# Kernel tuning notes

Measured on AMD Instinct MI355X. Metric: run time of the kernel, lower is better.

## Reference

```python
import jax, jax.numpy as jnp
import numpy as np

B = 524288
N = 5  # graph size hard-coded by reshape(batch, 5, 5) in the original
THRESHOLD = 0.85


def build_graph(x):
    # x: [B, N]. Row j of sample b is x[b] if x[b, j] != 0 else (1 - x[b]).
    # The torch code reads the condition from detached numpy values, so the
    # condition carries no gradient -> stop_gradient here.
    cond = jax.lax.stop_gradient(x)[:, :, None] != 0          # [B, N, 1]
    mat = jnp.where(cond, x[:, None, :], (1.0 - x)[:, None, :])  # [B, N, N]
    mat = mat * 2.0 - 1.0
    # subtract diag_embed(diagonal) -> zero the diagonal
    diag = jnp.einsum('bii->bi', mat)                         # [B, N]
    eye = jnp.eye(N, dtype=mat.dtype)
    return mat - diag[:, :, None] * eye[None]


def calculate_laplacian(adj):
    # Faithful to the original (buggy) torch.diag on a [B, N] matrix:
    # it extracts the length-N main diagonal of (column-sums - 1), which
    # then broadcasts over the LAST axis of adj.
    s = jnp.sum(adj, axis=1) - 1.0                            # [B, N]
    deg = jnp.diagonal(s)                                     # [N] (needs B >= N)
    return deg - adj                                          # [B, N, N]


def select_best_k(ev):
    # ev: complex [B, N]. energy_k = |mean_b(sum_{j<k} ev / sum_j ev)|;
    # return smallest k with energy > THRESHOLD, else N.
    total = jnp.sum(ev, axis=1)                               # [B] complex
    cums = jnp.cumsum(ev, axis=1)                             # [B, N] complex
    energies = jnp.abs(jnp.mean(cums / total[:, None], axis=0))  # [N] real
    exceeded = energies > THRESHOLD
    return jnp.where(jnp.any(exceeded), jnp.argmax(exceeded) + 1, N)


def setup_inputs() -> dict:
    key = jax.random.key(0)
    k1, k2 = jax.random.split(key)
    y_true = jax.random.randint(k1, (B, N), 0, 2).astype(jnp.float32)
    y_pred = jax.random.uniform(k2, (B, N), dtype=jnp.float32)
    return {"y_true": y_true, "y_pred": y_pred}


def reference(y_true, y_pred):
    graph_pred = build_graph(y_pred)
    graph_true = build_graph(y_true)
    lap_pred = calculate_laplacian(graph_pred)
    lap_true = calculate_laplacian(graph_true)
    ev_pred = jnp.linalg.eigvals(lap_pred)                    # [B, N] complex64
    ev_true = jnp.linalg.eigvals(lap_true)
    min_k = jnp.minimum(select_best_k(ev_pred), select_best_k(ev_true))
    # slice [:, :min_k] expressed as a static-shape mask (jit-safe)
    col_mask = jnp.arange(N) < min_k                          # [N] bool
    diff = jnp.where(col_mask[None, :], ev_pred - ev_true, 0.0 + 0.0j)
    # torch.norm on complex = Frobenius norm = sqrt(sum |.|^2), real scalar
    distance = jnp.sqrt(jnp.sum(jnp.abs(diff) ** 2))
    return distance  # torch.mean of a scalar is the scalar
```

## Files before the change

### kernel.cpp

```cpp
#include <hip/hip_runtime.h>
#include <math.h>


#define DEV __device__ __forceinline__

static DEV float slapy2f(float x, float y){
#pragma clang fp contract(off)
  float xa = fabsf(x), ya = fabsf(y);
  float w = fmaxf(xa, ya), z = fminf(xa, ya);
  if (z == 0.f) return w;
  float r = z / w;
  return w * sqrtf(1.f + r*r);
}

template<int LS>
static DEV float slarfg_col(int n, float* alpha, float* x){
#pragma clang fp contract(off)
  if (n <= 1) return 0.f;
  int m = n - 1;
  float xnorm;
  if (m == 1) xnorm = fabsf(x[0]);
  else {
    float scl = 0.f, ssq = 1.f;
    for (int i = 0; i < m; ++i){
      float xi = x[i*LS];
      if (xi != 0.f){
        float ax = fabsf(xi);
        if (scl < ax){ float r = scl/ax; ssq = 1.f + ssq*(r*r); scl = ax; }
        else         { float r = ax/scl; ssq = ssq + r*r; }
      }
    }
    xnorm = scl * sqrtf(ssq);
  }
  if (xnorm == 0.f) return 0.f;
  float a = *alpha;
  float beta = -copysignf(slapy2f(a, xnorm), a);
  float tau = (beta - a) / beta;
  float sc = 1.f / (a - beta);
  for (int i = 0; i < m; ++i) x[i*LS] *= sc;
  *alpha = beta;
  return tau;
}

static DEV float slarfg23(int nr, float* alpha, float* x1, float* x2){
#pragma clang fp contract(off)
  float xnorm;
  if (nr == 2) xnorm = fabsf(*x1);
  else {
    float scl = 0.f, ssq = 1.f;
    float v = *x1;
    if (v != 0.f){ float ax = fabsf(v); if (scl < ax){ float r=scl/ax; ssq=1.f+ssq*(r*r); scl=ax; } else { float r=ax/scl; ssq+=r*r; } }
    v = *x2;
    if (v != 0.f){ float ax = fabsf(v); if (scl < ax){ float r=scl/ax; ssq=1.f+ssq*(r*r); scl=ax; } else { float r=ax/scl; ssq+=r*r; } }
    xnorm = scl*sqrtf(ssq);
  }
  if (xnorm == 0.f) return 0.f;
  float a = *alpha;
  float beta = -copysignf(slapy2f(a, xnorm), a);
  float tau = (beta - a)/beta;
  float sc = 1.f/(a - beta);
  *x1 *= sc;
  if (nr == 3) *x2 *= sc;
  *alpha = beta;
  return tau;
}

static DEV void slanv2f(float a, float b, float c, float d,
                        float* rt1r, float* rt1i, float* rt2r, float* rt2i){
#pragma clang fp contract(off)
  const float eps = 1.1920929e-7f;
  if (c == 0.f){
  } else if (b == 0.f){
    float t = d; d = a; a = t; b = -c; c = 0.f;
  } else if ((a - d) == 0.f && copysignf(1.f,b) != copysignf(1.f,c)){
  } else {
    float temp = a - d;
    float p = 0.5f*temp;
    float bcmax = fmaxf(fabsf(b), fabsf(c));
    float bcmis = fminf(fabsf(b), fabsf(c)) * copysignf(1.f,b) * copysignf(1.f,c);
    float scale = fmaxf(fabsf(p), bcmax);
    float z = (p/scale)*p + (bcmax/scale)*bcmis;
    if (z >= 4.f*eps){
      z = p + copysignf(sqrtf(scale)*sqrtf(z), p);
      a = d + z;
      d = d - (bcmax/z)*bcmis;
      b = b - c;
      c = 0.f;
    } else {
      float sigma = b + c;
      float tau = slapy2f(sigma, temp);
      float cs = sqrtf(0.5f*(1.f + fabsf(sigma)/tau));
      float sn = -(p/(tau*cs))*copysignf(1.f, sigma);
      float aa = a*cs + b*sn,  bb = -a*sn + b*cs;
      float cc = c*cs + d*sn,  dd = -c*sn + d*cs;
      a = aa*cs + cc*sn;  b = bb*cs + dd*sn;
      c = -aa*sn + cc*cs; d = -bb*sn + dd*cs;
      temp = 0.5f*(a+d);
      a = temp; d = temp;
      if (c != 0.f){
        if (b != 0.f){
          if (copysignf(1.f,b) == copysignf(1.f,c)){
            float sab = sqrtf(fabsf(b)), sac = sqrtf(fabsf(c));
            p = copysignf(sab*sac, c);
            a = temp + p; d = temp - p;
            b = b - c; c = 0.f;
          }
        } else {
          b = -c; c = 0.f;
        }
      }
    }
  }
  *rt1r = a; *rt2r = d;
  if (c == 0.f){ *rt1i = 0.f; *rt2i = 0.f; }
  else { *rt1i = sqrtf(fabsf(b))*sqrtf(fabsf(c)); *rt2i = -(*rt1i); }
}

template<int LS>
static DEV void sgeev5(float* __restrict__ h){
#pragma clang fp contract(off)
#define A_(i,j) h[((((j)-1)*5 + ((i)-1)))*LS]
#define SETEV(p, vr, vi) do { int p_ = (p); float vr_ = (vr), vi_ = (vi); \
    h[(p_-1)*LS] = vr_; h[(5 + p_-1)*LS] = vi_; } while(0)
  const int n = 5;
  float scl1=1.f,scl2=1.f,scl3=1.f,scl4=1.f,scl5=1.f;

  int k = 1, l = 5;
  bool balDone = false;

  {
    bool again = true;
    while (again){
      again = false;
      for (int j = l; j >= 1; --j){
        bool iso = true;
        for (int i2 = 1; i2 <= l; ++i2){
          if (i2 == j) continue;
          if (A_(j,i2) != 0.f){ iso = false; break; }
        }
        if (iso){
          if (j != l){
            for (int r = 1; r <= l; ++r){ float t = A_(r,j); A_(r,j) = A_(r,l); A_(r,l) = t; }
            for (int c = k; c <= n; ++c){ float t = A_(j,c); A_(j,c) = A_(l,c); A_(l,c) = t; }
          }
          l -= 1;
          if (l == 1) balDone = true;
          else again = true;
          break;
        }
      }
      if (balDone) break;
    }
  }
  if (!balDone){
    bool again = true;
    while (again){
      again = false;
      for (int j = k; j <= l; ++j){
        bool iso = true;
        for (int i2 = k; i2 <= l; ++i2){
          if (i2 == j) continue;
          if (A_(i2,j) != 0.f){ iso = false; break; }
        }
        if (iso){
          if (j != k){
            for (int r = 1; r <= l; ++r){ float t = A_(r,j); A_(r,j) = A_(r,k); A_(r,k) = t; }
            for (int c = k; c <= n; ++c){ float t = A_(j,c); A_(j,c) = A_(k,c); A_(k,c) = t; }
          }
          k += 1;
          again = true;
          break;
        }
      }
    }
    const float sclfac = 2.f, factor = 0.95f;
    const float sfmin1 = 1.17549435e-38f / 1.1920929e-7f;
    const float sfmax1 = 1.f / sfmin1;
    const float sfmin2 = sfmin1 * sclfac;
    const float sfmax2 = 1.f / sfmin2;
    bool noconv = true;
    while (noconv){
      noconv = false;
      for (int i2 = k; i2 <= l; ++i2){
        float c = 0.f, r = 0.f;
        for (int j = k; j <= l; ++j){
          if (j == i2) continue;
          c += fabsf(A_(j,i2));
          r += fabsf(A_(i2,j));
        }
        float ca = 0.f; for (int rr = 1; rr <= l; ++rr) ca = fmaxf(ca, fabsf(A_(rr,i2)));
        float ra = 0.f; for (int cc = k; cc <= n; ++cc) ra = fmaxf(ra, fabsf(A_(i2,cc)));
        if (c == 0.f || r == 0.f) continue;
        float g = r / sclfac, f = 1.f, s = c + r;
        while (c < g){
          if (fmaxf(fmaxf(f,c),ca) >= sfmax2 || fminf(fminf(r,g),ra) <= sfmin2) break;
          f *= sclfac; c *= sclfac; ca *= sclfac; r /= sclfac; g /= sclfac; ra /= sclfac;
        }
        g = c / sclfac;
        while (g >= r){
          if (fmaxf(r,ra) >= sfmax2 || fminf(fminf(f,c),fminf(g,ca)) <= sfmin2) break;
          f /= sclfac; c /= sclfac; g /= sclfac; ca /= sclfac; r *= sclfac; ra *= sclfac;
        }
        if ((c + r) >= factor*s) continue;
        float s0 = (i2==1)?scl1:(i2==2)?scl2:(i2==3)?scl3:(i2==4)?scl4:scl5;
        if (f < 1.f && s0 < 1.f){ if (f*s0 <= sfmin1) continue; }
        if (f > 1.f && s0 > 1.f){ if (s0 >= sfmax1/f) continue; }
        float gg = 1.f/f;
        if      (i2==1) scl1 *= f;
        else if (i2==2) scl2 *= f;
        else if (i2==3) scl3 *= f;
        else if (i2==4) scl4 *= f;
        else            scl5 *= f;
        noconv = true;
        for (int cc = k; cc <= n; ++cc) A_(i2,cc) *= gg;
        for (int rr = 1; rr <= l; ++rr) A_(rr,i2) *= f;
      }
    }
  }
  const int ilo = k, ihi = l;

  for (int i2 = ilo; i2 <= ihi-1; ++i2){
    int nv = ihi - i2;
    int xrow = (i2+2 <= n) ? (i2+2) : n;
    float tau = slarfg_col<LS>(nv, &A_(i2+1, i2), &A_(xrow, i2));
    float aii = A_(i2+1, i2);
    A_(i2+1, i2) = 1.f;
    if (tau != 0.f){
      for (int row = 1; row <= ihi; ++row){
        float w = 0.f;
        for (int c2 = 1; c2 <= nv; ++c2) w += A_(row, i2+c2) * A_(i2+c2, i2);
        for (int c2 = 1; c2 <= nv; ++c2){
          float temp = (-tau) * A_(i2+c2, i2);
          A_(row, i2+c2) += w * temp;
        }
      }
      for (int c2 = i2+1; c2 <= n; ++c2){
        float w = 0.f;
        for (int r2 = 1; r2 <= nv; ++r2) w += A_(i2+r2, c2) * A_(i2+r2, i2);
        float temp = (-tau) * w;
        for (int r2 = 1; r2 <= nv; ++r2) A_(i2+r2, c2) += A_(i2+r2, i2) * temp;
      }
    }
    A_(i2+1, i2) = aii;
  }

  for (int p = 1; p <= ilo-1; ++p){ float v = A_(p,p); SETEV(p, v, 0.f); }
  for (int p = ihi+1; p <= n; ++p){ float v = A_(p,p); SETEV(p, v, 0.f); }

  if (ilo == ihi){
    float v = A_(ilo, ilo);
    SETEV(ilo, v, 0.f);
  } else {
    for (int j = ilo; j <= ihi-3; ++j){ A_(j+2, j) = 0.f; A_(j+3, j) = 0.f; }
    if (ilo <= ihi-2) A_(ihi, ihi-2) = 0.f;
    const int nh = ihi - ilo + 1;
    const float ulp = 1.1920929e-7f;
    const float smlnum = 1.17549435e-38f * ((float)nh / ulp);
    const int itmax = 30 * (nh > 10 ? nh : 10);
    int kdefl = 0;
    int i = ihi;
    while (i >= ilo){
      int l1 = ilo;
      bool conv = false;
      for (int its = 0; its <= itmax && !conv; ++its){
        int kk;
        for (kk = i; kk >= l1+1; --kk){
          float hk = fabsf(A_(kk, kk-1));
          if (hk <= smlnum) break;
          float tst = fabsf(A_(kk-1,kk-1)) + fabsf(A_(kk,kk));
          if (tst == 0.f){
            if (kk-2 >= ilo) tst += fabsf(A_(kk-1, kk-2));
            if (kk+1 <= ihi) tst += fabsf(A_(kk+1, kk));
          }
          if (hk <= ulp*tst){
            float ab = fmaxf(fabsf(A_(kk,kk-1)), fabsf(A_(kk-1,kk)));
            float ba = fminf(fabsf(A_(kk,kk-1)), fabsf(A_(kk-1,kk)));
            float aa = fmaxf(fabsf(A_(kk,kk)), fabsf(A_(kk-1,kk-1) - A_(kk,kk)));
            float bb = fminf(fabsf(A_(kk,kk)), fabsf(A_(kk-1,kk-1) - A_(kk,kk)));
            float s = aa + ab;
            if (ba*(ab/s) <= fmaxf(smlnum, ulp*(bb*(aa/s)))) break;
          }
        }
        l1 = kk;
        if (l1 > ilo) A_(l1, l1-1) = 0.f;
        if (l1 >= i-1){ conv = true; break; }
        kdefl++;
        float h11,h12,h21,h22;
        if (kdefl % 20 == 0){
          float s = fabsf(A_(i,i-1)) + fabsf(A_(i-1,i-2));
          h11 = 0.75f*s + A_(i,i); h12 = -0.4375f*s; h21 = s; h22 = h11;
        } else if (kdefl % 10 == 0){
          float s = fabsf(A_(l1+1,l1)) + fabsf(A_(l1+2,l1+1));
          h11 = 0.75f*s + A_(l1,l1); h12 = -0.4375f*s; h21 = s; h22 = h11;
        } else {
          h11 = A_(i-1,i-1); h21 = A_(i,i-1); h12 = A_(i-1,i); h22 = A_(i,i);
        }
        float s = fabsf(h11)+fabsf(h12)+fabsf(h21)+fabsf(h22);
        float rt1r, rt1i, rt2r, rt2i;
        if (s == 0.f){ rt1r = rt1i = rt2r = rt2i = 0.f; }
        else {
          h11 /= s; h21 /= s; h12 /= s; h22 /= s;
          float tr = (h11 + h22)/2.f;
          float det = (h11 - tr)*(h22 - tr) - h12*h21;
          float rtdisc = sqrtf(fabsf(det));
          if (det >= 0.f){
            rt1r = tr*s; rt2r = rt1r; rt1i = rtdisc*s; rt2i = -rt1i;
          } else {
            rt1r = tr + rtdisc; rt2r = tr - rtdisc;
            if (fabsf(rt1r - h22) <= fabsf(rt2r - h22)){ rt1r *= s; rt2r = rt1r; }
            else { rt2r *= s; rt1r = rt2r; }
            rt1i = 0.f; rt2i = 0.f;
          }
        }
        int m;
        float v1 = 0.f, v2 = 0.f, v3 = 0.f;
        for (m = i-2; m >= l1; --m){
          float h21s = A_(m+1, m);
          float s2 = fabsf(A_(m,m) - rt2r) + fabsf(rt2i) + fabsf(h21s);
          h21s = A_(m+1,m) / s2;
          v1 = h21s*A_(m, m+1) + (A_(m,m) - rt1r)*((A_(m,m) - rt2r)/s2) - rt1i*(rt2i/s2);
          v2 = h21s*(A_(m,m) + A_(m+1,m+1) - rt1r - rt2r);
          v3 = h21s*A_(m+2, m+1);
          float s3 = fabsf(v1) + fabsf(v2) + fabsf(v3);
          v1 /= s3; v2 /= s3; v3 /= s3;
          if (m == l1) break;
          if (fabsf(A_(m, m-1))*(fabsf(v2)+fabsf(v3)) <=
              ulp*fabsf(v1)*(fabsf(A_(m-1,m-1)) + fabsf(A_(m,m)) + fabsf(A_(m+1,m+1)))) break;
        }
        for (int kq = m; kq <= i-1; ++kq){
          int nr = (i - kq + 1 < 3) ? (i - kq + 1) : 3;
          float vv1, vv2, vv3 = 0.f;
          if (kq > m){
            vv1 = A_(kq, kq-1); vv2 = A_(kq+1, kq-1);
            if (nr == 3) vv3 = A_(kq+2, kq-1);
          } else { vv1 = v1; vv2 = v2; vv3 = v3; }
          float t1 = slarfg23(nr, &vv1, &vv2, &vv3);
          if (kq > m){
            A_(kq, kq-1) = vv1;
            A_(kq+1, kq-1) = 0.f;
            if (kq < i-1) A_(kq+2, kq-1) = 0.f;
          } else if (m > l1){
            A_(kq, kq-1) = A_(kq, kq-1)*(1.f - t1);
          }
          float v2r = vv2, t2 = t1*v2r;
          if (nr == 3){
            float v3r = vv3, t3 = t1*v3r;
            for (int j = kq; j <= i; ++j){
              float sum = A_(kq,j) + v2r*A_(kq+1,j) + v3r*A_(kq+2,j);
              A_(kq,j)   -= sum*t1;
              A_(kq+1,j) -= sum*t2;
              A_(kq+2,j) -= sum*t3;
            }
            int jhi = (kq+3 < i) ? (kq+3) : i;
            for (int j = l1; j <= jhi; ++j){
              float sum = t1*A_(j,kq) + t2*A_(j,kq+1) + t3*A_(j,kq+2);
              A_(j,kq)   -= sum;
              A_(j,kq+1) -= sum*v2r;
              A_(j,kq+2) -= sum*v3r;
            }
          } else {
            for (int j = kq; j <= i; ++j){
              float sum = A_(kq,j) + v2r*A_(kq+1,j);
              A_(kq,j)   -= sum*t1;
              A_(kq+1,j) -= sum*t2;
            }
            for (int j = l1; j <= i; ++j){
              float sum = t1*A_(j,kq) + t2*A_(j,kq+1);
              A_(j,kq)   -= sum;
              A_(j,kq+1) -= sum*v2r;
            }
          }
        }
      }
      if (l1 == i){
        float v = A_(i,i);
        SETEV(i, v, 0.f);
      } else if (l1 == i-1){
        float a11 = A_(i-1,i-1), a12 = A_(i-1,i);
        float a21 = A_(i,i-1),   a22 = A_(i,i);
        float r1r,r1i,r2r,r2i;
        slanv2f(a11, a12, a21, a22, &r1r, &r1i, &r2r, &r2i);
        SETEV(i-1, r1r, r1i);
        SETEV(i,   r2r, r2i);
      } else {
        float v = A_(i,i);
        SETEV(i, v, 0.f);
        l1 = i;
      }
      kdefl = 0;
      i = l1 - 1;
    }
  }
#undef SETEV
#undef A_
}

__global__ __launch_bounds__(64) void eig_init(const float* __restrict__ yt,
                                               const float* __restrict__ yp,
                                               float* __restrict__ misc,
                                               unsigned int* __restrict__ hist)
{
#pragma clang fp contract(off)
  __shared__ float sm[25];
  const int t = threadIdx.x;
  const int pat = blockIdx.x;
  if (pat == 0){
    if (t < 32) hist[t] = 0;
    if (t < 5){
      float xp[5], xt[5];
      for (int j = 0; j < 5; ++j){ xp[j] = yp[t*5+j]; xt[j] = yt[t*5+j]; }
      float cs = 0.f;
      for (int i = 0; i < 5; ++i){
        bool ci = (xp[i] != 0.f);
        float base = ci ? xp[t] : (1.f - xp[t]);
        float m2 = 2.f*base - 1.f;
        cs += (i == t) ? 0.f : m2;
      }
      misc[t] = cs - 1.f;
      float cs2 = 0.f;
      for (int i = 0; i < 5; ++i){
        bool ci = (xt[i] != 0.f);
        float base = ci ? xt[t] : (1.f - xt[t]);
        float m2 = 2.f*base - 1.f;
        cs2 += (i == t) ? 0.f : m2;
      }
      misc[5 + t] = cs2 - 1.f;
    }
  }
  if (t == 0){
    float degT[5];
    #pragma unroll
    for (int r = 0; r < 5; ++r){
      float xr[5];
      #pragma unroll
      for (int j = 0; j < 5; ++j) xr[j] = yt[r*5+j];
      float cs2 = 0.f;
      #pragma unroll
      for (int i = 0; i < 5; ++i){
        bool ci = (xr[i] != 0.f);
        float base = ci ? xr[r] : (1.f - xr[r]);
        float m2 = 2.f*base - 1.f;
        cs2 += (i == r) ? 0.f : m2;
      }
      degT[r] = cs2 - 1.f;
    }
    float xv[5];
    #pragma unroll
    for (int j = 0; j < 5; ++j) xv[j] = ((pat >> j) & 1) ? 1.f : 0.f;
    #pragma unroll
    for (int i = 0; i < 5; ++i){
      bool ci = (xv[i] != 0.f);
      #pragma unroll
      for (int j = 0; j < 5; ++j){
        float base = ci ? xv[j] : (1.f - xv[j]);
        float m2 = 2.f*base - 1.f;
        float adj = (i == j) ? 0.f : m2;
        sm[j*5 + i] = degT[j] - adj;
      }
    }
    sgeev5<1>(sm);
    float er[5], ei[5];
    #pragma unroll
    for (int kx = 0; kx < 5; ++kx){ er[kx] = sm[kx]; ei[kx] = sm[5+kx]; }
    float tr = 0.f, ti = 0.f;
    #pragma unroll
    for (int kx = 0; kx < 5; ++kx){ tr += er[kx]; ti += ei[kx]; }
    float den = tr*tr + ti*ti;
    float cr = 0.f, cii = 0.f;
    #pragma unroll
    for (int kx = 0; kx < 5; ++kx){
      misc[10 + pat*10 + 2*kx]     = er[kx];
      misc[10 + pat*10 + 2*kx + 1] = ei[kx];
      cr += er[kx]; cii += ei[kx];
      misc[330 + pat*10 + 2*kx]     = (cr*tr + cii*ti)/den;
      misc[330 + pat*10 + 2*kx + 1] = (cii*tr - cr*ti)/den;
    }
  }
}

__global__ __launch_bounds__(256, 6) void eig_main(const float* __restrict__ yt,
                                                   const float* __restrict__ yp,
                                                   double* __restrict__ partials,
                                                   unsigned int* __restrict__ hist,
                                                   const float* __restrict__ misc,
                                                   int nb)
{
#pragma clang fp contract(off)
  __shared__ float sm[25*256];
  __shared__ double red[4][16];
  __shared__ unsigned int hloc[32];
  const int tid = threadIdx.x;
  const int b = blockIdx.x*256 + tid;
  if (tid < 32) hloc[tid] = 0;
  __syncthreads();

  double vals[15];
  #pragma unroll
  for (int q = 0; q < 15; ++q) vals[q] = 0.0;

  if (b < nb){
    float* h = &sm[tid];
    float x[5];
    #pragma unroll
    for (int j = 0; j < 5; ++j) x[j] = yp[b*5 + j];
    float degp[5];
    #pragma unroll
    for (int j = 0; j < 5; ++j) degp[j] = misc[j];
    #pragma unroll
    for (int i = 0; i < 5; ++i){
      const bool ci = (x[i] != 0.f);
      #pragma unroll
      for (int j = 0; j < 5; ++j){
        float base = ci ? x[j] : (1.f - x[j]);
        float m2 = 2.f*base - 1.f;
        float adj = (i == j) ? 0.f : m2;
        h[(j*5 + i)*256] = degp[j] - adj;
      }
    }
    sgeev5<256>(h);
    float er[5], ei[5];
    #pragma unroll
    for (int kx = 0; kx < 5; ++kx){ er[kx] = h[kx*256]; ei[kx] = h[(5+kx)*256]; }
    float tr = 0.f, ti = 0.f;
    #pragma unroll
    for (int kx = 0; kx < 5; ++kx){ tr += er[kx]; ti += ei[kx]; }
    float den = tr*tr + ti*ti;
    float cr = 0.f, cii = 0.f;
    #pragma unroll
    for (int kx = 0; kx < 5; ++kx){
      cr += er[kx]; cii += ei[kx];
      float qr = (cr*tr + cii*ti)/den;
      float qi = (cii*tr - cr*ti)/den;
      vals[2*kx]   = (double)qr;
      vals[2*kx+1] = (double)qi;
    }
    int p = 0;
    #pragma unroll
    for (int j = 0; j < 5; ++j){ if (yt[b*5 + j] != 0.f) p |= (1 << j); }
    #pragma unroll
    for (int kx = 0; kx < 5; ++kx){
      float dr = er[kx] - misc[10 + p*10 + 2*kx];
      float di = ei[kx] - misc[10 + p*10 + 2*kx + 1];
      vals[10 + kx] = (double)dr*(double)dr + (double)di*(double)di;
    }
    atomicAdd(&hloc[p], 1u);
  }

  const int lane = tid & 63, wid = tid >> 6;
  #pragma unroll
  for (int q = 0; q < 15; ++q){
    double v = vals[q];
    #pragma unroll
    for (int off = 32; off >= 1; off >>= 1) v += __shfl_down(v, off, 64);
    if (lane == 0) red[wid][q] = v;
  }
  __syncthreads();
  if (tid == 0){
    #pragma unroll
    for (int q = 0; q < 15; ++q)
      partials[(size_t)blockIdx.x*15 + q] = red[0][q] + red[1][q] + red[2][q] + red[3][q];
  }
  if (tid < 32){
    unsigned int cv = hloc[tid];
    if (cv) atomicAdd(&hist[tid], cv);
  }
}

__global__ __launch_bounds__(256) void eig_final(const double* __restrict__ partials,
                                                 const unsigned int* __restrict__ hist,
                                                 const float* __restrict__ misc,
                                                 float* __restrict__ out,
                                                 int nb, int nblk)
{
#pragma clang fp contract(off)
  __shared__ double r2[4][16];
  const int tid = threadIdx.x;
  double acc[15];
  #pragma unroll
  for (int q = 0; q < 15; ++q) acc[q] = 0.0;
  for (int ib = tid; ib < nblk; ib += 256){
    #pragma unroll
    for (int q = 0; q < 15; ++q) acc[q] += partials[(size_t)ib*15 + q];
  }
  const int lane = tid & 63, wid = tid >> 6;
  #pragma unroll
  for (int q = 0; q < 15; ++q){
    double v = acc[q];
    #pragma unroll
    for (int off = 32; off >= 1; off >>= 1) v += __shfl_down(v, off, 64);
    if (lane == 0) r2[wid][q] = v;
  }
  __syncthreads();
  if (tid == 0){
    double tot[15];
    for (int q = 0; q < 15; ++q) tot[q] = r2[0][q] + r2[1][q] + r2[2][q] + r2[3][q];
    const double Bd = (double)nb;
    int kp = 5;
    for (int kx = 0; kx < 5; ++kx){
      double re = tot[2*kx]/Bd, im = tot[2*kx+1]/Bd;
      double e = sqrt(re*re + im*im);
      if (e > 0.85){ kp = kx + 1; break; }
    }
    int kt = 5;
    for (int kx = 0; kx < 5; ++kx){
      double re = 0.0, im = 0.0;
      for (int p = 0; p < 32; ++p){
        double cnt = (double)hist[p];
        re += cnt * (double)misc[330 + p*10 + 2*kx];
        im += cnt * (double)misc[330 + p*10 + 2*kx + 1];
      }
      re /= Bd; im /= Bd;
      double e = sqrt(re*re + im*im);
      if (e > 0.85){ kt = kx + 1; break; }
    }
    int mink = (kp < kt) ? kp : kt;
    double d2 = 0.0;
    for (int j = 0; j < mink; ++j) d2 += tot[10 + j];
    out[0] = (float)sqrt(d2);
  }
}

extern "C" void kernel_launch(void* const* d_in, const int* in_sizes, int n_in,
                              void* d_out, int out_size, void* d_ws, size_t ws_size,
                              hipStream_t stream)
{
  const float* yt = (const float*)d_in[0];
  const float* yp = (const float*)d_in[1];
  float* out = (float*)d_out;
  const int nb = in_sizes[0] / 5;
  const int nblk = (nb + 255) / 256;

  char* ws = (char*)d_ws;
  double* partials = (double*)ws;
  size_t off = (size_t)nblk * 15 * sizeof(double);
  off = (off + 255) & ~(size_t)255;
  unsigned int* hist = (unsigned int*)(ws + off);
  float* misc = (float*)(ws + off + 256);

  eig_init<<<32, 64, 0, stream>>>(yt, yp, misc, hist);
  eig_main<<<nblk, 256, 0, stream>>>(yt, yp, partials, hist, misc, nb);
  eig_final<<<1, 256, 0, stream>>>(partials, hist, misc, out, nb, nblk);
}
```

Before: 303.6 us.

## Unify QR bulge-chase reflector path, halve block size, store float partials

Merges the 2-element and 3-element Householder paths of the double-shift QR sweep into one 3-element path. When only two rows remain, the third row index is clamped and its coefficient is zero, which removes divergent branches inside the wavefront. The eigen kernel block size drops from 256 to 128 threads, halving per-block shared memory so more blocks fit per CU. Per-block partial sums are now stored as float instead of double, which reduces precision of the intermediate reduction. The clamped third row also adds redundant arithmetic in the 2-row case.

Result: no change. 307.8 us (+1.4%).

```diff
diff --git a/kernel.cpp b/kernel.cpp
--- a/kernel.cpp
+++ b/kernel.cpp
@@ -42,25 +42,21 @@
   return tau;
 }
 
-static DEV float slarfg23(int nr, float* alpha, float* x1, float* x2){
-#pragma clang fp contract(off)
-  float xnorm;
-  if (nr == 2) xnorm = fabsf(*x1);
-  else {
-    float scl = 0.f, ssq = 1.f;
-    float v = *x1;
-    if (v != 0.f){ float ax = fabsf(v); if (scl < ax){ float r=scl/ax; ssq=1.f+ssq*(r*r); scl=ax; } else { float r=ax/scl; ssq+=r*r; } }
-    v = *x2;
-    if (v != 0.f){ float ax = fabsf(v); if (scl < ax){ float r=scl/ax; ssq=1.f+ssq*(r*r); scl=ax; } else { float r=ax/scl; ssq+=r*r; } }
-    xnorm = scl*sqrtf(ssq);
-  }
+static DEV float slarfg3(float* alpha, float* x1, float* x2){
+#pragma clang fp contract(off)
+  float scl = 0.f, ssq = 1.f;
+  float v = *x1;
+  if (v != 0.f){ float ax = fabsf(v); if (scl < ax){ float r=scl/ax; ssq=1.f+ssq*(r*r); scl=ax; } else { float r=ax/scl; ssq+=r*r; } }
+  v = *x2;
+  if (v != 0.f){ float ax = fabsf(v); if (scl < ax){ float r=scl/ax; ssq=1.f+ssq*(r*r); scl=ax; } else { float r=ax/scl; ssq+=r*r; } }
+  float xnorm = scl*sqrtf(ssq);
   if (xnorm == 0.f) return 0.f;
   float a = *alpha;
   float beta = -copysignf(slapy2f(a, xnorm), a);
   float tau = (beta - a)/beta;
   float sc = 1.f/(a - beta);
   *x1 *= sc;
-  if (nr == 3) *x2 *= sc;
+  *x2 *= sc;
   *alpha = beta;
   return tau;
 }
@@ -328,13 +324,12 @@
               ulp*fabsf(v1)*(fabsf(A_(m-1,m-1)) + fabsf(A_(m,m)) + fabsf(A_(m+1,m+1)))) break;
         }
         for (int kq = m; kq <= i-1; ++kq){
-          int nr = (i - kq + 1 < 3) ? (i - kq + 1) : 3;
-          float vv1, vv2, vv3 = 0.f;
+          float vv1, vv2, vv3;
           if (kq > m){
             vv1 = A_(kq, kq-1); vv2 = A_(kq+1, kq-1);
-            if (nr == 3) vv3 = A_(kq+2, kq-1);
+            vv3 = (kq < i-1) ? A_(kq+2, kq-1) : 0.f;
           } else { vv1 = v1; vv2 = v2; vv3 = v3; }
-          float t1 = slarfg23(nr, &vv1, &vv2, &vv3);
+          float t1 = slarfg3(&vv1, &vv2, &vv3);
           if (kq > m){
             A_(kq, kq-1) = vv1;
             A_(kq+1, kq-1) = 0.f;
@@ -343,32 +338,20 @@
             A_(kq, kq-1) = A_(kq, kq-1)*(1.f - t1);
           }
           float v2r = vv2, t2 = t1*v2r;
-          if (nr == 3){
-            float v3r = vv3, t3 = t1*v3r;
-            for (int j = kq; j <= i; ++j){
-              float sum = A_(kq,j) + v2r*A_(kq+1,j) + v3r*A_(kq+2,j);
-              A_(kq,j)   -= sum*t1;
-              A_(kq+1,j) -= sum*t2;
-              A_(kq+2,j) -= sum*t3;
-            }
-            int jhi = (kq+3 < i) ? (kq+3) : i;
-            for (int j = l1; j <= jhi; ++j){
-              float sum = t1*A_(j,kq) + t2*A_(j,kq+1) + t3*A_(j,kq+2);
-              A_(j,kq)   -= sum;
-              A_(j,kq+1) -= sum*v2r;
-              A_(j,kq+2) -= sum*v3r;
-            }
-          } else {
-            for (int j = kq; j <= i; ++j){
-              float sum = A_(kq,j) + v2r*A_(kq+1,j);
-              A_(kq,j)   -= sum*t1;
-              A_(kq+1,j) -= sum*t2;
-            }
-            for (int j = l1; j <= i; ++j){
-              float sum = t1*A_(j,kq) + t2*A_(j,kq+1);
-              A_(j,kq)   -= sum;
-              A_(j,kq+1) -= sum*v2r;
-            }
+          float v3r = vv3, t3 = t1*v3r;
+          int r3 = (kq+2 <= i) ? (kq+2) : i;
+          for (int j = kq; j <= i; ++j){
+            float sum = A_(kq,j) + v2r*A_(kq+1,j) + v3r*A_(r3,j);
+            A_(kq,j)   -= sum*t1;
+            A_(kq+1,j) -= sum*t2;
+            A_(r3,j)   -= sum*t3;
+          }
+          int jhi = (kq+3 < i) ? (kq+3) : i;
+          for (int j = l1; j <= jhi; ++j){
+            float sum = t1*A_(j,kq) + t2*A_(j,kq+1) + t3*A_(j,r3);
+            A_(j,kq)   -= sum;
+            A_(j,kq+1) -= sum*v2r;
+            A_(j,r3)   -= sum*v3r;
           }
         }
       }
@@ -478,19 +461,19 @@
   }
 }
 
-__global__ __launch_bounds__(256, 6) void eig_main(const float* __restrict__ yt,
+__global__ __launch_bounds__(128, 6) void eig_main(const float* __restrict__ yt,
                                                    const float* __restrict__ yp,
-                                                   double* __restrict__ partials,
+                                                   float* __restrict__ partials,
                                                    unsigned int* __restrict__ hist,
                                                    const float* __restrict__ misc,
                                                    int nb)
 {
 #pragma clang fp contract(off)
-  __shared__ float sm[25*256];
-  __shared__ double red[4][16];
+  __shared__ float sm[25*128];
+  __shared__ double red[2][16];
   __shared__ unsigned int hloc[32];
   const int tid = threadIdx.x;
-  const int b = blockIdx.x*256 + tid;
+  const int b = blockIdx.x*128 + tid;
   if (tid < 32) hloc[tid] = 0;
   __syncthreads();
 
@@ -514,13 +497,13 @@
         float base = ci ? x[j] : (1.f - x[j]);
         float m2 = 2.f*base - 1.f;
         float adj = (i == j) ? 0.f : m2;
-        h[(j*5 + i)*256] = degp[j] - adj;
-      }
-    }
-    sgeev5<256>(h);
+        h[(j*5 + i)*128] = degp[j] - adj;
+      }
+    }
+    sgeev5<128>(h);
     float er[5], ei[5];
     #pragma unroll
-    for (int kx = 0; kx < 5; ++kx){ er[kx] = h[kx*256]; ei[kx] = h[(5+kx)*256]; }
+    for (int kx = 0; kx < 5; ++kx){ er[kx] = h[kx*128]; ei[kx] = h[(5+kx)*128]; }
     float tr = 0.f, ti = 0.f;
     #pragma unroll
     for (int kx = 0; kx < 5; ++kx){ tr += er[kx]; ti += ei[kx]; }
@@ -558,7 +541,7 @@
   if (tid == 0){
     #pragma unroll
     for (int q = 0; q < 15; ++q)
-      partials[(size_t)blockIdx.x*15 + q] = red[0][q] + red[1][q] + red[2][q] + red[3][q];
+      partials[(size_t)blockIdx.x*15 + q] = (float)(red[0][q] + red[1][q]);
   }
   if (tid < 32){
     unsigned int cv = hloc[tid];
@@ -566,7 +549,7 @@
   }
 }
 
-__global__ __launch_bounds__(256) void eig_final(const double* __restrict__ partials,
+__global__ __launch_bounds__(256) void eig_final(const float* __restrict__ partials,
                                                  const unsigned int* __restrict__ hist,
                                                  const float* __restrict__ misc,
                                                  float* __restrict__ out,
@@ -580,7 +563,7 @@
   for (int q = 0; q < 15; ++q) acc[q] = 0.0;
   for (int ib = tid; ib < nblk; ib += 256){
     #pragma unroll
-    for (int q = 0; q < 15; ++q) acc[q] += partials[(size_t)ib*15 + q];
+    for (int q = 0; q < 15; ++q) acc[q] += (double)partials[(size_t)ib*15 + q];
   }
   const int lane = tid & 63, wid = tid >> 6;
   #pragma unroll
@@ -628,16 +611,16 @@
   const float* yp = (const float*)d_in[1];
   float* out = (float*)d_out;
   const int nb = in_sizes[0] / 5;
-  const int nblk = (nb + 255) / 256;
+  const int nblk = (nb + 127) / 128;
 
   char* ws = (char*)d_ws;
-  double* partials = (double*)ws;
-  size_t off = (size_t)nblk * 15 * sizeof(double);
+  float* partials = (float*)ws;
+  size_t off = (size_t)nblk * 15 * sizeof(float);
   off = (off + 255) & ~(size_t)255;
   unsigned int* hist = (unsigned int*)(ws + off);
   float* misc = (float*)(ws + off + 256);
 
   eig_init<<<32, 64, 0, stream>>>(yt, yp, misc, hist);
-  eig_main<<<nblk, 256, 0, stream>>>(yt, yp, partials, hist, misc, nb);
+  eig_main<<<nblk, 128, 0, stream>>>(yt, yp, partials, hist, misc, nb);
   eig_final<<<1, 256, 0, stream>>>(partials, hist, misc, out, nb, nblk);
 }
```
